# Performance work log

Measured on AMD Instinct MI355X. Metric: run time of the kernel, lower is better.

Reference implementation:

```python
import jax, jax.numpy as jnp
import numpy as np

T, B, D = 160, 640, 40      # time-major frames, batch (N_spk*M_utt), log-mel dim
H, P, L = 768, 256, 3       # nb_hidden, nb_proj, nb_layers


def setup_inputs() -> dict:
    key = jax.random.key(0)
    ks = jax.random.split(key, 1 + 3 * L)
    inp = {"x": jax.random.normal(ks[0], (T, B, D), jnp.float32)}
    din = D
    for l in range(L):
        gs = np.float32(np.sqrt(2.0 / (din + P + 4 * H)))  # glorot-ish scale
        inp[f"W{l}"] = jax.random.normal(ks[1 + 3 * l], (din + P, 4 * H), jnp.float32) * gs
        inp[f"b{l}"] = jnp.zeros((4 * H,), jnp.float32)
        ps = np.float32(np.sqrt(2.0 / (H + P)))
        inp[f"Wp{l}"] = jax.random.normal(ks[3 + 3 * l], (H, P), jnp.float32) * ps
        din = P
    return inp


def lstmp_layer(x, W, b, Wp):
    # x: [T, B, d_in] time-major. TF LSTMCell with num_proj: state h has dim P,
    # gate order (i, j, f, o), forget_bias = 1.0.
    bsz = x.shape[1]
    c0 = jnp.zeros((bsz, H), x.dtype)
    h0 = jnp.zeros((bsz, P), x.dtype)

    def step(carry, xt):
        c, h = carry
        z = jnp.concatenate([xt, h], axis=-1) @ W + b            # [B, 4H]
        i, j, f, o = jnp.split(z, 4, axis=-1)
        c = jax.nn.sigmoid(f + 1.0) * c + jax.nn.sigmoid(i) * jnp.tanh(j)
        h = (jax.nn.sigmoid(o) * jnp.tanh(c)) @ Wp               # projection -> [B, P]
        return (c, h), h

    _, ys = jax.lax.scan(step, (c0, h0), x)                      # ys: [T, B, P]
    return ys


def reference(x, W0, b0, Wp0, W1, b1, Wp1, W2, b2, Wp2):
    h = lstmp_layer(x, W0, b0, Wp0)
    h = lstmp_layer(h, W1, b1, Wp1)
    h = lstmp_layer(h, W2, b2, Wp2)
    emb = h[-1]                                                  # last timestep: [B, P]
    return emb / (jnp.linalg.norm(emb, axis=-1, keepdims=True) + 1e-6)
```

## Files before the change

### kernel.cpp

```cpp
#include <hip/hip_runtime.h>
#include <hip/hip_bf16.h>

typedef __attribute__((ext_vector_type(4))) float f32x4;
typedef __attribute__((ext_vector_type(8))) short s16x8;

#define DEVFN static __device__ __forceinline__

#define TT  160
#define BB  640
#define DD  40
#define HH  768
#define PP  256
#define G4H 3072

#define NWG   192
#define NTHR  256

#define KH  256
#define KX0 64

#define STW1 328
#define STW2 520
#define STP  776
#define LDS_ELEMS 66560

#define XP_BYTES   (TT*BB*64*2)
#define HR_BYTES   (3*4*BB*PP*2)
#define SB_BYTES   (3*4*BB*HH*2)
#define XP_OFF     0
#define HR_OFF     (XP_OFF + XP_BYTES)
#define SB_OFF     (HR_OFF + HR_BYTES)
#define SYNC_OFF   (SB_OFF + SB_BYTES)
#define SYNC_BYTES 4096

DEVFN float sigm(float v)  { return __fdividef(1.f, 1.f + __expf(-v)); }
DEVFN float tanh_(float v) { return 2.f * __fdividef(1.f, 1.f + __expf(-2.f * v)) - 1.f; }
DEVFN f32x4 f4zero() { f32x4 v; v[0]=0.f; v[1]=0.f; v[2]=0.f; v[3]=0.f; return v; }

DEVFN void gst_b16(__hip_bfloat16* p, __hip_bfloat16 v) {
  unsigned short u = __builtin_bit_cast(unsigned short, v);
  asm volatile("global_store_short %0, %1, off sc0 sc1" :: "v"(p), "v"(u));
}

DEVFN unsigned ld_cc(const unsigned* p) {
  unsigned v;
  asm volatile("global_load_dword %0, %1, off sc0 sc1\n\ts_waitcnt vmcnt(0)"
               : "=v"(v) : "v"(p) : "memory");
  return v;
}
DEVFN void st_cc(unsigned* p, unsigned v) {
  asm volatile("global_store_dword %0, %1, off sc0 sc1" :: "v"(p), "v"(v) : "memory");
}
DEVFN void ld3_cc(const unsigned* p0, const unsigned* p1, const unsigned* p2,
                  unsigned& a, unsigned& b, unsigned& c) {
  asm volatile("global_load_dword %0, %3, off sc0 sc1\n\t"
               "global_load_dword %1, %4, off sc0 sc1\n\t"
               "global_load_dword %2, %5, off sc0 sc1\n\t"
               "s_waitcnt vmcnt(0)"
               : "=&v"(a), "=&v"(b), "=&v"(c)
               : "v"(p0), "v"(p1), "v"(p2) : "memory");
}

DEVFN void fence_acq() { __builtin_amdgcn_fence(__ATOMIC_ACQUIRE, "agent"); }

#define SFLAG(s,l,g) ((s) + 256 + ((l)*48+(g))*4)
#define PFLAG(s,l,p) ((s) + 832 + ((l)*16+(p))*4)

DEVFN void init_barrier(unsigned* sync, int bid, int tid) {
  __syncthreads();
  if (tid == 0) st_cc(sync + bid, 1u);
  if (tid < 64) {
    unsigned a, b, c;
    for (;;) {
      ld3_cc(sync + tid, sync + 64 + tid, sync + 128 + tid, a, b, c);
      if (__all((a >= 1u) & (b >= 1u) & (c >= 1u))) break;
    }
    fence_acq();
  }
  __syncthreads();
}

DEVFN void wait_flags(const unsigned* base, int nf, int thr, int tid, bool dofence) {
  if (thr <= 0) return;
  if (tid < 64) {
    const unsigned* p = base + tid * 4;
    for (;;) {
      int v = (tid < nf) ? (int)ld_cc(p) : 0x7fffffff;
      if (__all(v >= thr)) break;
    }
    if (dofence) fence_acq();
  }
  __syncthreads();
}

DEVFN void wait_proj(const unsigned* sf_l, const unsigned* sf_lp1, int has2,
                     int thr1, int thr2, int tid, bool dofence) {
  if (tid < 64) {
    const unsigned* p1 = sf_l + tid * 4;
    const unsigned* p2 = sf_lp1 + tid * 4;
    for (;;) {
      int v1 = (tid < 24) ? (int)ld_cc(p1) : 0x7fffffff;
      int v2 = (has2 && tid < 24 && thr2 > 0) ? (int)ld_cc(p2) : 0x7fffffff;
      if (__all((v1 >= thr1) & (v2 >= thr2))) break;
    }
    if (dofence) fence_acq();
  }
  __syncthreads();
}

DEVFN void set_flag(unsigned* p, unsigned v, int tid) {
  __syncthreads();
  if (tid == 0) st_cc(p, v);
}

__global__ __launch_bounds__(NTHR, 1)
void lstmp_persistent(const float* __restrict__ xin,
                      const float* __restrict__ W0, const float* __restrict__ b0, const float* __restrict__ Wp0,
                      const float* __restrict__ W1, const float* __restrict__ b1, const float* __restrict__ Wp1,
                      const float* __restrict__ W2, const float* __restrict__ b2, const float* __restrict__ Wp2,
                      float* __restrict__ outp, unsigned char* __restrict__ ws)
{
  __shared__ __align__(16) __hip_bfloat16 lds[LDS_ELEMS];

  const int bid  = blockIdx.x;
  const int tid  = threadIdx.x;
  const int lane = tid & 63;
  const int wave = tid >> 6;
  const int q    = lane >> 4;
  const int c16  = lane & 15;

  __hip_bfloat16* Xp = (__hip_bfloat16*)(ws + XP_OFF);
  __hip_bfloat16* Hr = (__hip_bfloat16*)(ws + HR_OFF);
  __hip_bfloat16* Sb = (__hip_bfloat16*)(ws + SB_OFF);
  unsigned* sync     = (unsigned*)(ws + SYNC_OFF);

  const int xcd  = bid & 7;
  const int slot = bid >> 3;
  const bool isGate = (xcd < 6);
  int l = 0, bc = 0, hg = 0, mt = 0, nt = 0;
  if (isGate) { l = xcd >> 1; bc = xcd & 1; hg = slot; }
  else        { l = slot >> 3; int r = slot & 7; mt = (xcd - 6) * 2 + (r >> 2); nt = r & 3; }

  const int KX  = (l == 0) ? KX0 : 256;
  const int KT  = KX + KH;
  const int STW = (l == 0) ? STW1 : STW2;

  const float* Wl  = (l == 0) ? W0  : ((l == 1) ? W1  : W2);
  const float* bl  = (l == 0) ? b0  : ((l == 1) ? b1  : b2);
  const float* Wpl = (l == 0) ? Wp0 : ((l == 1) ? Wp1 : Wp2);

  for (int e = bid * NTHR + tid; e < TT * BB * 64; e += NWG * NTHR) {
    int k  = e & 63;
    int tb = e >> 6;
    float v = (k < DD) ? xin[(size_t)tb * DD + k] : 0.f;
    gst_b16(&Xp[e], __float2bfloat16(v));
  }

  if (isGate) {
    for (int idx = tid; idx < 128 * KT; idx += NTHR) {
      int kk = idx >> 7;
      int nn = idx & 127;
      int col = (nn >> 5) * HH + hg * 32 + (nn & 31);
      float v;
      if (l == 0) {
        v = (kk < DD) ? Wl[(size_t)kk * G4H + col]
                      : ((kk < KX0) ? 0.f : Wl[(size_t)(kk - 24) * G4H + col]);
      } else {
        v = Wl[(size_t)kk * G4H + col];
      }
      lds[nn * STW + kk] = __float2bfloat16(v);
    }
  } else {
    for (int idx = tid; idx < 64 * HH; idx += NTHR) {
      int kk = idx >> 6;
      int nn = idx & 63;
      lds[nn * STP + kk] = __float2bfloat16(Wpl[(size_t)kk * PP + nt * 64 + nn]);
    }
  }

  init_barrier(sync, bid, tid);

  if (isGate) {
    const int gid = bc * 24 + hg;
    unsigned* myflag = SFLAG(sync, l, gid);
    const unsigned* pf_own = PFLAG(sync, l, bc * 8);
    const unsigned* pf_prv = (l > 0) ? PFLAG(sync, l - 1, bc * 8) : PFLAG(sync, l, bc * 8);

    const int wmg = wave >> 1, wng = wave & 1;
    const int m0g = bc * 320 + wmg * 160;
    const int hcl = wng * 16 + c16;
    float biasv[4];
#pragma unroll
    for (int g = 0; g < 4; ++g) biasv[g] = bl[g * HH + hg * 32 + hcl];

    f32x4 acc[10][4];
    float cst[10][4];
#pragma unroll
    for (int mi = 0; mi < 10; ++mi)
#pragma unroll
      for (int g = 0; g < 4; ++g) { acc[mi][g] = f4zero(); cst[mi][g] = 0.f; }

    auto gate_gemm = [&](const __hip_bfloat16* A, int lda, int kbase, int klen) {
      s16x8 avA[5], avB[5];
#pragma unroll
      for (int mi = 0; mi < 5; ++mi)
        avA[mi] = *(const s16x8*)(A + (size_t)(m0g + mi * 16 + c16) * lda + 8 * q);
#pragma unroll 1
      for (int ks = 0; ks < klen; ks += 32) {
#pragma unroll
        for (int mi = 0; mi < 5; ++mi)
          avB[mi] = *(const s16x8*)(A + (size_t)(m0g + (5 + mi) * 16 + c16) * lda + ks + 8 * q);
        s16x8 bv[4];
#pragma unroll
        for (int g = 0; g < 4; ++g)
          bv[g] = *(const s16x8*)(lds + (g * 32 + hcl) * STW + kbase + ks + 8 * q);
#pragma unroll
        for (int mi = 0; mi < 5; ++mi)
#pragma unroll
          for (int g = 0; g < 4; ++g)
            acc[mi][g] = __builtin_amdgcn_mfma_f32_16x16x32_bf16(avA[mi], bv[g], acc[mi][g], 0, 0, 0);
        if (ks + 32 < klen) {
#pragma unroll
          for (int mi = 0; mi < 5; ++mi)
            avA[mi] = *(const s16x8*)(A + (size_t)(m0g + mi * 16 + c16) * lda + ks + 32 + 8 * q);
        }
#pragma unroll
        for (int mi = 0; mi < 5; ++mi)
#pragma unroll
          for (int g = 0; g < 4; ++g)
            acc[5 + mi][g] = __builtin_amdgcn_mfma_f32_16x16x32_bf16(avB[mi], bv[g], acc[5 + mi][g], 0, 0, 0);
      }
    };

    auto gate_update = [&](int t) {
      __hip_bfloat16* S = Sb + ((size_t)l * 4 + ((unsigned)t & 3)) * BB * HH;
#pragma unroll
      for (int mi = 0; mi < 10; ++mi) {
#pragma unroll
        for (int r = 0; r < 4; ++r) {
          float iv = acc[mi][0][r] + biasv[0];
          float jv = acc[mi][1][r] + biasv[1];
          float fv = acc[mi][2][r] + biasv[2];
          float ov = acc[mi][3][r] + biasv[3];
          float c  = sigm(fv + 1.f) * cst[mi][r] + sigm(iv) * tanh_(jv);
          cst[mi][r] = c;
          float sv = sigm(ov) * tanh_(c);
          gst_b16(&S[(size_t)(m0g + mi * 16 + q * 4 + r) * HH + hg * 32 + hcl],
                  __float2bfloat16(sv));
        }
#pragma unroll
        for (int g = 0; g < 4; ++g) acc[mi][g] = f4zero();
      }
    };

    if (l == 0) gate_gemm(Xp, 64, 0, KX0);
    else {
      wait_flags(pf_prv, 8, 1, tid, true);
      gate_gemm(Hr + ((size_t)(l - 1) * 4 + 1) * BB * PP, PP, 0, 256);
    }

    for (int t = 0; t < TT; ++t) {
      wait_flags(pf_own, 8, t, tid, (t & 3) == 0);
      gate_gemm(Hr + ((size_t)l * 4 + ((unsigned)t & 3)) * BB * PP, PP, KX, KH);
      gate_update(t);
      set_flag(myflag, (unsigned)(t + 1), tid);
      if (t + 1 < TT) {
        if (l == 0) gate_gemm(Xp + (size_t)(t + 1) * BB * 64, 64, 0, KX0);
        else {
          wait_flags(pf_prv, 8, t + 2, tid, false);
          gate_gemm(Hr + ((size_t)(l - 1) * 4 + ((unsigned)(t + 2) & 3)) * BB * PP, PP, 0, 256);
        }
      }
    }
  } else {
    const int pid = mt * 4 + nt;
    const int bch = mt >> 1;
    unsigned* myflag = PFLAG(sync, l, pid);
    const unsigned* sf_own = SFLAG(sync, l, bch * 24);
    const unsigned* sf_nxt = (l < 2) ? SFLAG(sync, l + 1, bch * 24) : SFLAG(sync, l, bch * 24);
    const int m0p = mt * 160 + (wave >> 1) * 80;
    const int np0 = (wave & 1) * 32;

    for (int t = 0; t < TT; ++t) {
      wait_proj(sf_own, sf_nxt, l < 2 ? 1 : 0, t + 1, t - 3, tid, (t & 3) == 0);

      const __hip_bfloat16* A = Sb + ((size_t)l * 4 + ((unsigned)t & 3)) * BB * HH;
      const __hip_bfloat16* ab[5];
#pragma unroll
      for (int mi = 0; mi < 5; ++mi)
        ab[mi] = A + (size_t)(m0p + mi * 16 + c16) * HH + 8 * q;

      f32x4 pa[5][2];
#pragma unroll
      for (int mi = 0; mi < 5; ++mi) { pa[mi][0] = f4zero(); pa[mi][1] = f4zero(); }

      s16x8 r0[5], r1[5], r2[5], r3[5];
#pragma unroll
      for (int mi = 0; mi < 5; ++mi) {
        r0[mi] = *(const s16x8*)(ab[mi] + 0);
        r1[mi] = *(const s16x8*)(ab[mi] + 32);
        r2[mi] = *(const s16x8*)(ab[mi] + 64);
        r3[mi] = *(const s16x8*)(ab[mi] + 96);
      }

#define PSLICE(RB, S)                                                          \
      {                                                                        \
        s16x8 bv0 = *(const s16x8*)(lds + (np0 + c16) * STP + (S) * 32 + 8 * q);      \
        s16x8 bv1 = *(const s16x8*)(lds + (np0 + 16 + c16) * STP + (S) * 32 + 8 * q); \
        _Pragma("unroll")                                                      \
        for (int mi = 0; mi < 5; ++mi) {                                       \
          pa[mi][0] = __builtin_amdgcn_mfma_f32_16x16x32_bf16(RB[mi], bv0, pa[mi][0], 0, 0, 0); \
          pa[mi][1] = __builtin_amdgcn_mfma_f32_16x16x32_bf16(RB[mi], bv1, pa[mi][1], 0, 0, 0); \
        }                                                                      \
        if ((S) + 4 < 24) {                                                    \
          _Pragma("unroll")                                                    \
          for (int mi = 0; mi < 5; ++mi)                                       \
            RB[mi] = *(const s16x8*)(ab[mi] + ((S) + 4) * 32);                 \
        }                                                                      \
      }

      PSLICE(r0, 0)  PSLICE(r1, 1)  PSLICE(r2, 2)  PSLICE(r3, 3)
      PSLICE(r0, 4)  PSLICE(r1, 5)  PSLICE(r2, 6)  PSLICE(r3, 7)
      PSLICE(r0, 8)  PSLICE(r1, 9)  PSLICE(r2, 10) PSLICE(r3, 11)
      PSLICE(r0, 12) PSLICE(r1, 13) PSLICE(r2, 14) PSLICE(r3, 15)
      PSLICE(r0, 16) PSLICE(r1, 17) PSLICE(r2, 18) PSLICE(r3, 19)
      PSLICE(r0, 20) PSLICE(r1, 21) PSLICE(r2, 22) PSLICE(r3, 23)
#undef PSLICE

      __hip_bfloat16* Hd = Hr + ((size_t)l * 4 + ((unsigned)(t + 1) & 3)) * BB * PP;
#pragma unroll
      for (int mi = 0; mi < 5; ++mi)
#pragma unroll
        for (int ni = 0; ni < 2; ++ni)
#pragma unroll
          for (int r = 0; r < 4; ++r)
            gst_b16(&Hd[(size_t)(m0p + mi * 16 + q * 4 + r) * PP + nt * 64 + np0 + ni * 16 + c16],
                    __float2bfloat16(pa[mi][ni][r]));

      set_flag(myflag, (unsigned)(t + 1), tid);
    }
  }

  wait_flags(PFLAG(sync, 2, 0), 16, TT, tid, true);
  const __hip_bfloat16* hf = Hr + (size_t)(2 * 4 + 0) * BB * PP;
  float* red = reinterpret_cast<float*>(lds);
  for (int row = bid; row < BB; row += NWG) {
    float v = __bfloat162float(hf[(size_t)row * PP + tid]);
    float ssq = v * v;
#pragma unroll
    for (int off = 32; off > 0; off >>= 1) ssq += __shfl_down(ssq, off, 64);
    if (lane == 0) red[wave] = ssq;
    __syncthreads();
    float tot = red[0] + red[1] + red[2] + red[3];
    outp[(size_t)row * PP + tid] = v * __fdividef(1.f, sqrtf(tot) + 1e-6f);
    __syncthreads();
  }
}

extern "C" void kernel_launch(void* const* d_in, const int* in_sizes, int n_in,
                              void* d_out, int out_size, void* d_ws, size_t ws_size,
                              hipStream_t stream) {
  (void)in_sizes; (void)n_in; (void)out_size; (void)ws_size;
  unsigned char* ws = (unsigned char*)d_ws;
  hipMemsetAsync(ws + HR_OFF, 0, HR_BYTES, stream);
  hipMemsetAsync(ws + SYNC_OFF, 0, SYNC_BYTES, stream);
  lstmp_persistent<<<dim3(NWG), dim3(NTHR), 0, stream>>>(
      (const float*)d_in[0],
      (const float*)d_in[1], (const float*)d_in[2], (const float*)d_in[3],
      (const float*)d_in[4], (const float*)d_in[5], (const float*)d_in[6],
      (const float*)d_in[7], (const float*)d_in[8], (const float*)d_in[9],
      (float*)d_out, ws);
}
```

Before: 5.427 ms.

## Double workgroup size so gate waves split rows and halve accumulator registers

Raises the block size from 256 to 512 threads. Each gate wave now owns 80 batch rows instead of 160, which halves its accumulator and cell-state register arrays, and the k-loop is restructured to consume two 32-wide slices per iteration. In projection workgroups only the first four waves do the work while the extra waves idle apart from flag handling, and the final normalisation processes two rows per block. The aim is more waves in flight and lower register pressure on the serial recurrent critical path, at the cost of more threads taking part in barrier and flag synchronisation.

```diff
diff --git a/kernel.cpp b/kernel.cpp
--- a/kernel.cpp
+++ b/kernel.cpp
@@ -14,7 +14,7 @@
 #define G4H 3072
 
 #define NWG   192
-#define NTHR  256
+#define NTHR  512
 
 #define KH  256
 #define KX0 64
@@ -187,55 +187,59 @@
     const unsigned* pf_prv = (l > 0) ? PFLAG(sync, l - 1, bc * 8) : PFLAG(sync, l, bc * 8);
 
     const int wmg = wave >> 1, wng = wave & 1;
-    const int m0g = bc * 320 + wmg * 160;
+    const int m0g = bc * 320 + wmg * 80;
     const int hcl = wng * 16 + c16;
     float biasv[4];
 #pragma unroll
     for (int g = 0; g < 4; ++g) biasv[g] = bl[g * HH + hg * 32 + hcl];
 
-    f32x4 acc[10][4];
-    float cst[10][4];
-#pragma unroll
-    for (int mi = 0; mi < 10; ++mi)
+    f32x4 acc[5][4];
+    float cst[5][4];
+#pragma unroll
+    for (int mi = 0; mi < 5; ++mi)
 #pragma unroll
       for (int g = 0; g < 4; ++g) { acc[mi][g] = f4zero(); cst[mi][g] = 0.f; }
 
     auto gate_gemm = [&](const __hip_bfloat16* A, int lda, int kbase, int klen) {
-      s16x8 avA[5], avB[5];
+      s16x8 a0[5], a1[5];
 #pragma unroll
       for (int mi = 0; mi < 5; ++mi)
-        avA[mi] = *(const s16x8*)(A + (size_t)(m0g + mi * 16 + c16) * lda + 8 * q);
+        a0[mi] = *(const s16x8*)(A + (size_t)(m0g + mi * 16 + c16) * lda + 8 * q);
 #pragma unroll 1
-      for (int ks = 0; ks < klen; ks += 32) {
-#pragma unroll
-        for (int mi = 0; mi < 5; ++mi)
-          avB[mi] = *(const s16x8*)(A + (size_t)(m0g + (5 + mi) * 16 + c16) * lda + ks + 8 * q);
+      for (int it2 = 0; it2 < klen / 64; ++it2) {
+        const int ks0 = it2 * 64, ks1 = ks0 + 32;
+#pragma unroll
+        for (int mi = 0; mi < 5; ++mi)
+          a1[mi] = *(const s16x8*)(A + (size_t)(m0g + mi * 16 + c16) * lda + ks1 + 8 * q);
         s16x8 bv[4];
 #pragma unroll
         for (int g = 0; g < 4; ++g)
-          bv[g] = *(const s16x8*)(lds + (g * 32 + hcl) * STW + kbase + ks + 8 * q);
+          bv[g] = *(const s16x8*)(lds + (g * 32 + hcl) * STW + kbase + ks0 + 8 * q);
 #pragma unroll
         for (int mi = 0; mi < 5; ++mi)
 #pragma unroll
           for (int g = 0; g < 4; ++g)
-            acc[mi][g] = __builtin_amdgcn_mfma_f32_16x16x32_bf16(avA[mi], bv[g], acc[mi][g], 0, 0, 0);
-        if (ks + 32 < klen) {
+            acc[mi][g] = __builtin_amdgcn_mfma_f32_16x16x32_bf16(a0[mi], bv[g], acc[mi][g], 0, 0, 0);
+        if (it2 + 1 < klen / 64) {
 #pragma unroll
           for (int mi = 0; mi < 5; ++mi)
-            avA[mi] = *(const s16x8*)(A + (size_t)(m0g + mi * 16 + c16) * lda + ks + 32 + 8 * q);
-        }
+            a0[mi] = *(const s16x8*)(A + (size_t)(m0g + mi * 16 + c16) * lda + ks0 + 64 + 8 * q);
+        }
+#pragma unroll
+        for (int g = 0; g < 4; ++g)
+          bv[g] = *(const s16x8*)(lds + (g * 32 + hcl) * STW + kbase + ks1 + 8 * q);
 #pragma unroll
         for (int mi = 0; mi < 5; ++mi)
 #pragma unroll
           for (int g = 0; g < 4; ++g)
-            acc[5 + mi][g] = __builtin_amdgcn_mfma_f32_16x16x32_bf16(avB[mi], bv[g], acc[5 + mi][g], 0, 0, 0);
+            acc[mi][g] = __builtin_amdgcn_mfma_f32_16x16x32_bf16(a1[mi], bv[g], acc[mi][g], 0, 0, 0);
       }
     };
 
     auto gate_update = [&](int t) {
       __hip_bfloat16* S = Sb + ((size_t)l * 4 + ((unsigned)t & 3)) * BB * HH;
 #pragma unroll
-      for (int mi = 0; mi < 10; ++mi) {
+      for (int mi = 0; mi < 5; ++mi) {
 #pragma unroll
         for (int r = 0; r < 4; ++r) {
           float iv = acc[mi][0][r] + biasv[0];
@@ -278,64 +282,66 @@
     unsigned* myflag = PFLAG(sync, l, pid);
     const unsigned* sf_own = SFLAG(sync, l, bch * 24);
     const unsigned* sf_nxt = (l < 2) ? SFLAG(sync, l + 1, bch * 24) : SFLAG(sync, l, bch * 24);
-    const int m0p = mt * 160 + (wave >> 1) * 80;
+    const int m0p = mt * 160 + ((wave & 3) >> 1) * 80;
     const int np0 = (wave & 1) * 32;
 
     for (int t = 0; t < TT; ++t) {
       wait_proj(sf_own, sf_nxt, l < 2 ? 1 : 0, t + 1, t - 3, tid, (t & 3) == 0);
 
-      const __hip_bfloat16* A = Sb + ((size_t)l * 4 + ((unsigned)t & 3)) * BB * HH;
-      const __hip_bfloat16* ab[5];
-#pragma unroll
-      for (int mi = 0; mi < 5; ++mi)
-        ab[mi] = A + (size_t)(m0p + mi * 16 + c16) * HH + 8 * q;
-
-      f32x4 pa[5][2];
-#pragma unroll
-      for (int mi = 0; mi < 5; ++mi) { pa[mi][0] = f4zero(); pa[mi][1] = f4zero(); }
-
-      s16x8 r0[5], r1[5], r2[5], r3[5];
-#pragma unroll
-      for (int mi = 0; mi < 5; ++mi) {
-        r0[mi] = *(const s16x8*)(ab[mi] + 0);
-        r1[mi] = *(const s16x8*)(ab[mi] + 32);
-        r2[mi] = *(const s16x8*)(ab[mi] + 64);
-        r3[mi] = *(const s16x8*)(ab[mi] + 96);
-      }
+      if (wave < 4) {
+        const __hip_bfloat16* A = Sb + ((size_t)l * 4 + ((unsigned)t & 3)) * BB * HH;
+        const __hip_bfloat16* ab[5];
+#pragma unroll
+        for (int mi = 0; mi < 5; ++mi)
+          ab[mi] = A + (size_t)(m0p + mi * 16 + c16) * HH + 8 * q;
+
+        f32x4 pa[5][2];
+#pragma unroll
+        for (int mi = 0; mi < 5; ++mi) { pa[mi][0] = f4zero(); pa[mi][1] = f4zero(); }
+
+        s16x8 r0[5], r1[5], r2[5], r3[5];
+#pragma unroll
+        for (int mi = 0; mi < 5; ++mi) {
+          r0[mi] = *(const s16x8*)(ab[mi] + 0);
+          r1[mi] = *(const s16x8*)(ab[mi] + 32);
+          r2[mi] = *(const s16x8*)(ab[mi] + 64);
+          r3[mi] = *(const s16x8*)(ab[mi] + 96);
+        }
 
 #define PSLICE(RB, S)                                                          \
-      {                                                                        \
-        s16x8 bv0 = *(const s16x8*)(lds + (np0 + c16) * STP + (S) * 32 + 8 * q);      \
-        s16x8 bv1 = *(const s16x8*)(lds + (np0 + 16 + c16) * STP + (S) * 32 + 8 * q); \
-        _Pragma("unroll")                                                      \
-        for (int mi = 0; mi < 5; ++mi) {                                       \
-          pa[mi][0] = __builtin_amdgcn_mfma_f32_16x16x32_bf16(RB[mi], bv0, pa[mi][0], 0, 0, 0); \
-          pa[mi][1] = __builtin_amdgcn_mfma_f32_16x16x32_bf16(RB[mi], bv1, pa[mi][1], 0, 0, 0); \
-        }                                                                      \
-        if ((S) + 4 < 24) {                                                    \
+        {                                                                      \
+          s16x8 bv0 = *(const s16x8*)(lds + (np0 + c16) * STP + (S) * 32 + 8 * q);      \
+          s16x8 bv1 = *(const s16x8*)(lds + (np0 + 16 + c16) * STP + (S) * 32 + 8 * q); \
           _Pragma("unroll")                                                    \
-          for (int mi = 0; mi < 5; ++mi)                                       \
-            RB[mi] = *(const s16x8*)(ab[mi] + ((S) + 4) * 32);                 \
-        }                                                                      \
-      }
-
-      PSLICE(r0, 0)  PSLICE(r1, 1)  PSLICE(r2, 2)  PSLICE(r3, 3)
-      PSLICE(r0, 4)  PSLICE(r1, 5)  PSLICE(r2, 6)  PSLICE(r3, 7)
-      PSLICE(r0, 8)  PSLICE(r1, 9)  PSLICE(r2, 10) PSLICE(r3, 11)
-      PSLICE(r0, 12) PSLICE(r1, 13) PSLICE(r2, 14) PSLICE(r3, 15)
-      PSLICE(r0, 16) PSLICE(r1, 17) PSLICE(r2, 18) PSLICE(r3, 19)
-      PSLICE(r0, 20) PSLICE(r1, 21) PSLICE(r2, 22) PSLICE(r3, 23)
+          for (int mi = 0; mi < 5; ++mi) {                                     \
+            pa[mi][0] = __builtin_amdgcn_mfma_f32_16x16x32_bf16(RB[mi], bv0, pa[mi][0], 0, 0, 0); \
+            pa[mi][1] = __builtin_amdgcn_mfma_f32_16x16x32_bf16(RB[mi], bv1, pa[mi][1], 0, 0, 0); \
+          }                                                                    \
+          if ((S) + 4 < 24) {                                                  \
+            _Pragma("unroll")                                                  \
+            for (int mi = 0; mi < 5; ++mi)                                     \
+              RB[mi] = *(const s16x8*)(ab[mi] + ((S) + 4) * 32);               \
+          }                                                                    \
+        }
+
+        PSLICE(r0, 0)  PSLICE(r1, 1)  PSLICE(r2, 2)  PSLICE(r3, 3)
+        PSLICE(r0, 4)  PSLICE(r1, 5)  PSLICE(r2, 6)  PSLICE(r3, 7)
+        PSLICE(r0, 8)  PSLICE(r1, 9)  PSLICE(r2, 10) PSLICE(r3, 11)
+        PSLICE(r0, 12) PSLICE(r1, 13) PSLICE(r2, 14) PSLICE(r3, 15)
+        PSLICE(r0, 16) PSLICE(r1, 17) PSLICE(r2, 18) PSLICE(r3, 19)
+        PSLICE(r0, 20) PSLICE(r1, 21) PSLICE(r2, 22) PSLICE(r3, 23)
 #undef PSLICE
 
-      __hip_bfloat16* Hd = Hr + ((size_t)l * 4 + ((unsigned)(t + 1) & 3)) * BB * PP;
-#pragma unroll
-      for (int mi = 0; mi < 5; ++mi)
-#pragma unroll
-        for (int ni = 0; ni < 2; ++ni)
-#pragma unroll
-          for (int r = 0; r < 4; ++r)
-            gst_b16(&Hd[(size_t)(m0p + mi * 16 + q * 4 + r) * PP + nt * 64 + np0 + ni * 16 + c16],
-                    __float2bfloat16(pa[mi][ni][r]));
+        __hip_bfloat16* Hd = Hr + ((size_t)l * 4 + ((unsigned)(t + 1) & 3)) * BB * PP;
+#pragma unroll
+        for (int mi = 0; mi < 5; ++mi)
+#pragma unroll
+          for (int ni = 0; ni < 2; ++ni)
+#pragma unroll
+            for (int r = 0; r < 4; ++r)
+              gst_b16(&Hd[(size_t)(m0p + mi * 16 + q * 4 + r) * PP + nt * 64 + np0 + ni * 16 + c16],
+                      __float2bfloat16(pa[mi][ni][r]));
+      }
 
       set_flag(myflag, (unsigned)(t + 1), tid);
     }
@@ -344,15 +350,18 @@
   wait_flags(PFLAG(sync, 2, 0), 16, TT, tid, true);
   const __hip_bfloat16* hf = Hr + (size_t)(2 * 4 + 0) * BB * PP;
   float* red = reinterpret_cast<float*>(lds);
-  for (int row = bid; row < BB; row += NWG) {
-    float v = __bfloat162float(hf[(size_t)row * PP + tid]);
+  const int half = tid >> 8;
+  const int col  = tid & 255;
+  for (int row0 = bid * 2; row0 < BB; row0 += NWG * 2) {
+    const int row = row0 + half;
+    float v = __bfloat162float(hf[(size_t)row * PP + col]);
     float ssq = v * v;
 #pragma unroll
     for (int off = 32; off > 0; off >>= 1) ssq += __shfl_down(ssq, off, 64);
     if (lane == 0) red[wave] = ssq;
     __syncthreads();
-    float tot = red[0] + red[1] + red[2] + red[3];
-    outp[(size_t)row * PP + tid] = v * __fdividef(1.f, sqrtf(tot) + 1e-6f);
+    float tot = red[half * 4 + 0] + red[half * 4 + 1] + red[half * 4 + 2] + red[half * 4 + 3];
+    outp[(size_t)row * PP + col] = v * __fdividef(1.f, sqrtf(tot) + 1e-6f);
     __syncthreads();
   }
 }
```

After: 5.335 ms. No clear change (-1.7%).
